# Performance work log

Hardware: AMD Instinct MI355X
Metric: run time of the kernel (lower is better)

The kernel has to match this reference:

```python
import jax, jax.numpy as jnp
import numpy as np

INPUT_DIM = 20000
UNITS = 4096
NNZ = 800000
BATCH = 1024


def setup_inputs() -> dict:
    key = jax.random.key(0)
    k1, k2, k3, k4 = jax.random.split(key, 4)
    x = jax.random.normal(k1, (BATCH, INPUT_DIM), dtype=jnp.float32)
    kernel_vector = jax.random.normal(k2, (NNZ,), dtype=jnp.float32) * 0.05
    bias = jnp.zeros((UNITS,), dtype=jnp.float32)
    rows = jax.random.randint(k3, (NNZ,), 0, INPUT_DIM, dtype=jnp.int32)
    cols = jax.random.randint(k4, (NNZ,), 0, UNITS, dtype=jnp.int32)
    nonzero_ind = jnp.stack([rows, cols], axis=1)  # [NNZ, 2]
    return {"x": x, "kernel_vector": kernel_vector, "bias": bias, "nonzero_ind": nonzero_ind}


def reference(x, kernel_vector, bias, nonzero_ind):
    # scatter_nd: build dense (input_dim, units) kernel; duplicates accumulate (matches tf.scatter_nd)
    input_dim = x.shape[1]
    units = bias.shape[0]
    dense_kernel = jnp.zeros((input_dim, units), dtype=kernel_vector.dtype)
    dense_kernel = dense_kernel.at[nonzero_ind[:, 0], nonzero_ind[:, 1]].add(kernel_vector)
    out = jnp.matmul(x, dense_kernel) + bias  # [B, units]
    return jnp.tanh(out)
```

## Files before the change

### kernel.cpp

```cpp
#include <hip/hip_runtime.h>
#include <hip/hip_fp16.h>

#define BATCH      1024
#define INPUT_DIM  20000
#define UNITS      4096
#define NNZ        800000
#define BAND_ROW   10000
#define CAP        192
#define NSLOT      (UNITS * 2)

#define WS_XT     0
#define WS_CNT    40960000
#define WS_PAIRS  (WS_CNT + 32768)
#define ZERO_INTS (NSLOT + NSLOT * CAP * 2)
#define ZERO_U4   (ZERO_INTS / 4)
#define SCAT_BLK  (NNZ / 256)
#define TR_BLK    ((INPUT_DIM / 32) * (BATCH / 64))

__global__ __launch_bounds__(256) void zero_kernel(uint4* __restrict__ z) {
    unsigned int gid = blockIdx.x * 256 + threadIdx.x;
    z[gid] = make_uint4(0u, 0u, 0u, 0u);
}

__global__ __launch_bounds__(256) void fused_prep_kernel(
    const int2* __restrict__ ind2, const float* __restrict__ vals_in,
    int* __restrict__ cnt, uint2* __restrict__ pairs,
    const float4* __restrict__ x4, unsigned int* __restrict__ xTu) {
    __shared__ float tile[64][33];
    int t = threadIdx.x;
    int bid = blockIdx.x;

    if (bid < SCAT_BLK) {
        int i = bid * 256 + t;
        int2 rc = ind2[i];
        int band = (rc.x >= BAND_ROW) ? 1 : 0;
        int slot = (rc.y << 1) + band;
        int pos = atomicAdd(&cnt[slot], 1);
        if (pos < CAP)
            pairs[slot * CAP + pos] =
                make_uint2((unsigned)rc.x << 11, __float_as_uint(vals_in[i]));
        return;
    }

    int tb = bid - SCAT_BLK;
    int d0 = (tb % 625) * 32;
    int b0 = (tb / 625) * 64;

    int fx = t & 7, rr = t >> 3;
#pragma unroll
    for (int p = 0; p < 2; p++) {
        int b = rr + p * 32;
        float4 v = x4[(size_t)(b0 + b) * (INPUT_DIM / 4) + (d0 >> 2) + fx];
        tile[b][fx * 4 + 0] = v.x; tile[b][fx * 4 + 1] = v.y;
        tile[b][fx * 4 + 2] = v.z; tile[b][fx * 4 + 3] = v.w;
    }
    __syncthreads();
    int bq = t & 15, dd = t >> 4;
#pragma unroll
    for (int p = 0; p < 2; p++) {
        int d = dd + p * 16;
        unsigned short h0 = __half_as_ushort(__float2half(tile[bq * 4 + 0][d]));
        unsigned short h1 = __half_as_ushort(__float2half(tile[bq * 4 + 1][d]));
        unsigned short h2 = __half_as_ushort(__float2half(tile[bq * 4 + 2][d]));
        unsigned short h3 = __half_as_ushort(__float2half(tile[bq * 4 + 3][d]));
        uint2 u = make_uint2((unsigned)h0 | ((unsigned)h1 << 16),
                             (unsigned)h2 | ((unsigned)h3 << 16));
        *(uint2*)(xTu + (size_t)(d0 + d) * (BATCH / 2) + (b0 >> 1) + bq * 2) = u;
    }
}

__device__ __forceinline__ void accum8(uint4 q, float v, float* a) {
    const unsigned* h = (const unsigned*)&q;
#pragma unroll
    for (int i = 0; i < 4; i++) {
        asm("v_fma_mix_f32 %0, %1, %2, %0 op_sel:[0,0,0] op_sel_hi:[1,0,0]"
            : "+v"(a[2 * i])     : "v"(h[i]), "v"(v));
        asm("v_fma_mix_f32 %0, %1, %2, %0 op_sel:[1,0,0] op_sel_hi:[1,0,0]"
            : "+v"(a[2 * i + 1]) : "v"(h[i]), "v"(v));
    }
}

__global__ __launch_bounds__(512, 8) void spmm_kernel(
    const uint2* __restrict__ pairs, const int* __restrict__ cnt,
    const char* __restrict__ xTb, const float* __restrict__ bias,
    float* __restrict__ out) {
    __shared__ uint2 spairs[32][CAP];
    float (*tile)[17] = reinterpret_cast<float(*)[17]>(&spairs[0][0]);

    int bid = blockIdx.x;
    int kLow = bid & 7;
    int cg = bid >> 3;
    int tid = threadIdx.x;
    int lane = tid & 63;
    int w = tid >> 6;
    int g = lane >> 4;
    int s = lane & 15;
    unsigned int laneterm = (unsigned)(kLow << 8) + (unsigned)(s << 4);
    int colbase = (cg << 4) + (w << 1);

    int base2 = colbase << 1;
    int4 c4 = *(const int4*)(cnt + base2);
    int ncnt[4] = {c4.x, c4.y, c4.z, c4.w};

    int npd[4];
#pragma unroll
    for (int k = 0; k < 4; ++k) {
        int n = ncnt[k];
        if (n > CAP) n = CAP;
        int npad = (n + 7) & ~7;
        npd[k] = npad;
        const uint2* src = pairs + (base2 + k) * CAP + lane;
        uint2* dst = &spairs[(w << 2) + k][lane];
        if (npad) {
            dst[0] = src[0];
            if (npad > 64)  dst[64]  = src[64];
            if (npad > 128) dst[128] = src[128];
        }
    }

    float a[2][8] = {{0.f,0.f,0.f,0.f,0.f,0.f,0.f,0.f},
                     {0.f,0.f,0.f,0.f,0.f,0.f,0.f,0.f}};
#pragma unroll
    for (int bd = 0; bd < 2; ++bd) {
#pragma unroll
        for (int c = 0; c < 2; ++c) {
            int k = 2 * c + bd;
            int npad = npd[k];
            if (npad == 0) continue;
            const uint2* pb = &spairs[(w << 2) + k][g];
            float* ac = a[c];
            uint2 e0 = pb[0];
            uint2 e1 = pb[4];
            for (int j = 0; j < npad; j += 8) {
                uint4 q0 = *(const uint4*)(xTb + (e0.x + laneterm));
                uint4 q1 = *(const uint4*)(xTb + (e1.x + laneterm));
                float v0 = __uint_as_float(e0.y);
                float v1 = __uint_as_float(e1.y);
                if (j + 8 < npad) {
                    e0 = pb[j + 8];
                    e1 = pb[j + 12];
                }
                accum8(q0, v0, ac);
                accum8(q1, v1, ac);
            }
        }
    }

    __syncthreads();

#pragma unroll
    for (int c = 0; c < 2; ++c) {
        float bc = bias[colbase + c];
#pragma unroll
        for (int i = 0; i < 8; i++) {
            float v = a[c][i];
            v += __shfl_xor(v, 16, 64);
            v += __shfl_xor(v, 32, 64);
            if (g == 0)
                tile[(s << 3) + i][(w << 1) + c] = tanhf(v + bc);
        }
    }
    __syncthreads();

    int bl = tid >> 2;
    int c0 = (tid & 3) << 2;
    float4 vv = make_float4(tile[bl][c0], tile[bl][c0 + 1],
                            tile[bl][c0 + 2], tile[bl][c0 + 3]);
    *(float4*)(out + (size_t)((kLow << 7) + bl) * UNITS + (cg << 4) + c0) = vv;
}

extern "C" void kernel_launch(void* const* d_in, const int* in_sizes, int n_in,
                              void* d_out, int out_size, void* d_ws, size_t ws_size,
                              hipStream_t stream) {
    const float* x    = (const float*)d_in[0];
    const float* vals = (const float*)d_in[1];
    const float* bias = (const float*)d_in[2];
    const int*   ind  = (const int*)d_in[3];
    float* out = (float*)d_out;

    char* ws = (char*)d_ws;
    char*  xT    = ws + WS_XT;
    int*   cnt   = (int*)(ws + WS_CNT);
    uint2* pairs = (uint2*)(ws + WS_PAIRS);

    zero_kernel<<<ZERO_U4 / 256, 256, 0, stream>>>((uint4*)(ws + WS_CNT));
    fused_prep_kernel<<<SCAT_BLK + TR_BLK, 256, 0, stream>>>(
        (const int2*)ind, vals, cnt, pairs, (const float4*)x, (unsigned int*)xT);
    spmm_kernel<<<2048, 512, 0, stream>>>(pairs, cnt, xT, bias, out);
}
```

Before: 262.6 us.

## Zero only counters, split staged pairs into row/value arrays, interleave column streams

```diff
diff --git a/kernel.cpp b/kernel.cpp
--- a/kernel.cpp
+++ b/kernel.cpp
@@ -12,14 +12,11 @@
 #define WS_XT     0
 #define WS_CNT    40960000
 #define WS_PAIRS  (WS_CNT + 32768)
-#define ZERO_INTS (NSLOT + NSLOT * CAP * 2)
-#define ZERO_U4   (ZERO_INTS / 4)
 #define SCAT_BLK  (NNZ / 256)
 #define TR_BLK    ((INPUT_DIM / 32) * (BATCH / 64))
 
 __global__ __launch_bounds__(256) void zero_kernel(uint4* __restrict__ z) {
-    unsigned int gid = blockIdx.x * 256 + threadIdx.x;
-    z[gid] = make_uint4(0u, 0u, 0u, 0u);
+    z[blockIdx.x * 256 + threadIdx.x] = make_uint4(0u, 0u, 0u, 0u);
 }
 
 __global__ __launch_bounds__(256) void fused_prep_kernel(
@@ -84,8 +81,9 @@
     const uint2* __restrict__ pairs, const int* __restrict__ cnt,
     const char* __restrict__ xTb, const float* __restrict__ bias,
     float* __restrict__ out) {
-    __shared__ uint2 spairs[32][CAP];
-    float (*tile)[17] = reinterpret_cast<float(*)[17]>(&spairs[0][0]);
+    __shared__ alignas(16) unsigned short srow[32][CAP];
+    __shared__ float sval[32][CAP];
+    float (*tile)[17] = reinterpret_cast<float(*)[17]>(&srow[0][0]);
 
     int bid = blockIdx.x;
     int kLow = bid & 7;
@@ -107,14 +105,22 @@
     for (int k = 0; k < 4; ++k) {
         int n = ncnt[k];
         if (n > CAP) n = CAP;
-        int npad = (n + 7) & ~7;
-        npd[k] = npad;
+        npd[k] = (n + 7) & ~7;
         const uint2* src = pairs + (base2 + k) * CAP + lane;
-        uint2* dst = &spairs[(w << 2) + k][lane];
-        if (npad) {
-            dst[0] = src[0];
-            if (npad > 64)  dst[64]  = src[64];
-            if (npad > 128) dst[128] = src[128];
+        int wsl = (w << 2) + k;
+#pragma unroll
+        for (int ch = 0; ch < 3; ++ch) {
+            int idx = ch * 64 + lane;
+            unsigned short r = 0; float v = 0.f;
+            if (ch * 64 < n) {
+                uint2 p = src[ch * 64];
+                if (idx < n) {
+                    r = (unsigned short)(p.x >> 11);
+                    v = __uint_as_float(p.y);
+                }
+            }
+            srow[wsl][idx] = r;
+            sval[wsl][idx] = v;
         }
     }
 
@@ -122,27 +128,34 @@
                      {0.f,0.f,0.f,0.f,0.f,0.f,0.f,0.f}};
 #pragma unroll
     for (int bd = 0; bd < 2; ++bd) {
-#pragma unroll
-        for (int c = 0; c < 2; ++c) {
-            int k = 2 * c + bd;
-            int npad = npd[k];
-            if (npad == 0) continue;
-            const uint2* pb = &spairs[(w << 2) + k][g];
-            float* ac = a[c];
-            uint2 e0 = pb[0];
-            uint2 e1 = pb[4];
-            for (int j = 0; j < npad; j += 8) {
-                uint4 q0 = *(const uint4*)(xTb + (e0.x + laneterm));
-                uint4 q1 = *(const uint4*)(xTb + (e1.x + laneterm));
-                float v0 = __uint_as_float(e0.y);
-                float v1 = __uint_as_float(e1.y);
-                if (j + 8 < npad) {
-                    e0 = pb[j + 8];
-                    e1 = pb[j + 12];
-                }
-                accum8(q0, v0, ac);
-                accum8(q1, v1, ac);
+        int npA = npd[bd];
+        int npB = npd[2 + bd];
+        int npm = npA > npB ? npA : npB;
+        if (npm == 0) continue;
+        int wA = (w << 2) + bd, wB = (w << 2) + 2 + bd;
+        const unsigned short* prA = &srow[wA][g];
+        const float*          pvA = &sval[wA][g];
+        const unsigned short* prB = &srow[wB][g];
+        const float*          pvB = &sval[wB][g];
+
+        unsigned int rA0 = prA[0], rA1 = prA[4], rB0 = prB[0], rB1 = prB[4];
+        float vA0 = pvA[0], vA1 = pvA[4], vB0 = pvB[0], vB1 = pvB[4];
+        for (int j = 0; j < npm; j += 8) {
+            uint4 qA0 = *(const uint4*)(xTb + ((rA0 << 11) + laneterm));
+            uint4 qA1 = *(const uint4*)(xTb + ((rA1 << 11) + laneterm));
+            uint4 qB0 = *(const uint4*)(xTb + ((rB0 << 11) + laneterm));
+            uint4 qB1 = *(const uint4*)(xTb + ((rB1 << 11) + laneterm));
+            float fA0 = vA0, fA1 = vA1, fB0 = vB0, fB1 = vB1;
+            if (j + 8 < npm) {
+                rA0 = prA[j + 8]; rA1 = prA[j + 12];
+                vA0 = pvA[j + 8]; vA1 = pvA[j + 12];
+                rB0 = prB[j + 8]; rB1 = prB[j + 12];
+                vB0 = pvB[j + 8]; vB1 = pvB[j + 12];
             }
+            accum8(qA0, fA0, a[0]);
+            accum8(qA1, fA1, a[0]);
+            accum8(qB0, fB0, a[1]);
+            accum8(qB1, fB1, a[1]);
         }
     }
 
@@ -183,7 +196,7 @@
     int*   cnt   = (int*)(ws + WS_CNT);
     uint2* pairs = (uint2*)(ws + WS_PAIRS);
 
-    zero_kernel<<<ZERO_U4 / 256, 256, 0, stream>>>((uint4*)(ws + WS_CNT));
+    zero_kernel<<<8, 256, 0, stream>>>((uint4*)(ws + WS_CNT));
     fused_prep_kernel<<<SCAT_BLK + TR_BLK, 256, 0, stream>>>(
         (const int2*)ind, vals, cnt, pairs, (const float4*)x, (unsigned int*)xT);
     spmm_kernel<<<2048, 512, 0, stream>>>(pairs, cnt, xT, bias, out);
```

Result: no change. 262.2 us (-0.2%).
